# Kernel tuning notes

Measured on AMD Instinct MI355X. Metric: run time of the kernel, lower is better.

Reference implementation:

```python
import jax, jax.numpy as jnp
import numpy as np

N_MODULES = 8
AG_HIDDEN = 512
N_HID = 512
OUT_SIZE = 10
BATCH = 8192


def _state_mask(n_modules, n0, n1):
    # torch: eye(M).repeat_interleave(n0, 0).repeat_interleave(n1, 1)
    m = jnp.eye(n_modules, dtype=jnp.float32)
    return jnp.repeat(jnp.repeat(m, n0, axis=0), n1, axis=1)


def setup_inputs() -> dict:
    key = jax.random.key(0)
    ks = jax.random.split(key, 5)
    d_in = N_MODULES * AG_HIDDEN
    d_hid = N_MODULES * N_HID
    d_out = N_MODULES * OUT_SIZE
    s1 = 1.0 / np.sqrt(d_in)
    s2 = 1.0 / np.sqrt(d_hid)
    return {
        "x": jax.random.normal(ks[0], (BATCH, d_in), jnp.float32),
        "W1": jax.random.uniform(ks[1], (d_hid, d_in), jnp.float32, -s1, s1),
        "b1": jax.random.uniform(ks[2], (d_hid,), jnp.float32, -s1, s1),
        "W2": jax.random.uniform(ks[3], (d_out, d_hid), jnp.float32, -s2, s2),
        "b2": jax.random.uniform(ks[4], (d_out,), jnp.float32, -s2, s2),
    }


def reference(x, W1, b1, W2, b2):
    # block-diagonal masks (intra-module connectivity only)
    mask1 = _state_mask(N_MODULES, N_HID, AG_HIDDEN)   # [d_hid, d_in]
    mask2 = _state_mask(N_MODULES, OUT_SIZE, N_HID)    # [d_out, d_hid]
    h = jax.nn.relu(x @ (W1 * mask1).T + b1)           # [B, d_hid]
    y = h @ (W2 * mask2).T + b2                        # [B, d_out]
    # split(OUT_SIZE, -1) then stack on dim 1 == reshape to [B, n_modules, OUT_SIZE]
    return y.reshape(y.shape[0], N_MODULES, OUT_SIZE)
```

## Files before the change

kernel.cpp:

```cpp
#include <hip/hip_runtime.h>


#define NMOD 8
#define DIM 512
#define OSZ 10
#define BATCH 8192
#define D_IN 4096
#define D_OUT 80
#define BM 128
#define BN 256
#define BK 32

#define ASTRIDE 40
#define HSTRIDE 264
#define LDSA_SZ 5120
#define LDSB_SZ 8192

typedef __attribute__((ext_vector_type(8))) short short8;
typedef __attribute__((ext_vector_type(4))) float float4v;

__device__ __forceinline__ unsigned short f2bf(float f) {
    unsigned int u = __builtin_bit_cast(unsigned int, f);
    u += 0x7fffu + ((u >> 16) & 1u);
    return (unsigned short)(u >> 16);
}

__device__ __forceinline__ short8 cvt8(float4 a, float4 b) {
    short8 r;
    r[0] = (short)f2bf(a.x); r[1] = (short)f2bf(a.y); r[2] = (short)f2bf(a.z); r[3] = (short)f2bf(a.w);
    r[4] = (short)f2bf(b.x); r[5] = (short)f2bf(b.y); r[6] = (short)f2bf(b.z); r[7] = (short)f2bf(b.w);
    return r;
}

__global__ void init_out_kernel(const float* __restrict__ b2, float* __restrict__ out) {
    int idx = blockIdx.x * 256 + threadIdx.x;
    out[idx] = b2[idx % D_OUT];
}

__global__ void cvt_w_kernel(const float* __restrict__ W1, ushort* __restrict__ w1b) {
    int j = blockIdx.x * 256 + threadIdx.x;
    int mm = j >> 16, rem = j & 65535, r = rem >> 7, c4 = rem & 127;
    float4 v = *(const float4*)(W1 + (size_t)(mm * DIM + r) * D_IN + mm * DIM + c4 * 4);
    *(ushort4*)(w1b + (size_t)mm * DIM * DIM + r * DIM + c4 * 4) =
        make_ushort4(f2bf(v.x), f2bf(v.y), f2bf(v.z), f2bf(v.w));
}

template <bool WPRE>
__global__ __launch_bounds__(256, 2)
void fused_kernel(const float* __restrict__ x, const float* __restrict__ W1,
                  const ushort* __restrict__ w1b, const float* __restrict__ b1,
                  const float* __restrict__ W2, const float* __restrict__ b2,
                  float* __restrict__ out) {
    __shared__ __attribute__((aligned(16))) ushort smem[26624];
    ushort* ldsA0 = smem;
    ushort* ldsA1 = smem + LDSA_SZ;
    ushort* ldsB0 = smem + 2 * LDSA_SZ;
    ushort* ldsB1 = smem + 2 * LDSA_SZ + LDSB_SZ;
    ushort* ldsH  = smem;

    const int tid  = threadIdx.x;
    const int wave = tid >> 6;
    const int lane = tid & 63;
    const int r16  = lane & 15;
    const int kq   = lane >> 4;

    const int bid     = blockIdx.x;
    const int m       = bid & 7;
    const int half    = (bid >> 3) & 1;
    const int rowBase = (bid >> 4) * BM;

    const float*  xsrc = x + (size_t)rowBase * D_IN + m * DIM;
    const ushort* w1h  = w1b + (size_t)m * DIM * DIM + (size_t)half * BN * DIM;
    const float*  w1f  = W1 + (size_t)(m * DIM + half * BN) * D_IN + m * DIM;

    const int arow = tid >> 1;
    const int ah   = tid & 1;
    const int brow = tid >> 2;
    const int bc   = tid & 3;

    float4v acc[8][4];
#pragma unroll
    for (int i = 0; i < 8; i++)
#pragma unroll
        for (int j = 0; j < 4; j++) acc[i][j] = (float4v){0.f, 0.f, 0.f, 0.f};

    if (WPRE) {
#pragma unroll
        for (int r = 0; r < 4; r++) {
            const int row = r * 64 + brow;
            const int f   = (row >> 1) & 3;
            __builtin_amdgcn_global_load_lds(
                (const __attribute__((address_space(1))) void*)(w1h + (size_t)row * DIM + (bc ^ f) * 8),
                (__attribute__((address_space(3))) void*)(ldsB0 + row * BK + bc * 8), 16, 0, 0);
        }
    } else {
#pragma unroll
        for (int r = 0; r < 4; r++) {
            const int row = r * 64 + brow;
            const int f   = (row >> 1) & 3;
            const float* p = w1f + (size_t)row * D_IN + bc * 8;
            *(short8*)(ldsB0 + row * BK + (bc ^ f) * 8) = cvt8(*(const float4*)p, *(const float4*)(p + 4));
        }
    }
    {
        const float* p = xsrc + (size_t)arow * D_IN + ah * 16;
        float4 a0 = *(const float4*)p, a1 = *(const float4*)(p + 4);
        float4 a2 = *(const float4*)(p + 8), a3 = *(const float4*)(p + 12);
        *(short8*)(ldsA0 + arow * ASTRIDE + ah * 16)     = cvt8(a0, a1);
        *(short8*)(ldsA0 + arow * ASTRIDE + ah * 16 + 8) = cvt8(a2, a3);
    }

    for (int kk = 0; kk < DIM / BK; kk++) {
        __syncthreads();
        ushort* Ac = (kk & 1) ? ldsA1 : ldsA0;
        ushort* Bc = (kk & 1) ? ldsB1 : ldsB0;
        ushort* An = (kk & 1) ? ldsA0 : ldsA1;
        ushort* Bn = (kk & 1) ? ldsB0 : ldsB1;

        float4 xr0, xr1, xr2, xr3;
        const bool pf = (kk < DIM / BK - 1);
        if (pf) {
            const int k0n = (kk + 1) * BK;
            if (WPRE) {
#pragma unroll
                for (int r = 0; r < 4; r++) {
                    const int row = r * 64 + brow;
                    const int f   = (row >> 1) & 3;
                    __builtin_amdgcn_global_load_lds(
                        (const __attribute__((address_space(1))) void*)(w1h + (size_t)row * DIM + k0n + (bc ^ f) * 8),
                        (__attribute__((address_space(3))) void*)(Bn + row * BK + bc * 8), 16, 0, 0);
                }
            }
            const float* p = xsrc + (size_t)arow * D_IN + kk * BK + BK + ah * 16;
            xr0 = *(const float4*)p;     xr1 = *(const float4*)(p + 4);
            xr2 = *(const float4*)(p + 8); xr3 = *(const float4*)(p + 12);
        }

        short8 aF[8], bF[4];
#pragma unroll
        for (int mt = 0; mt < 8; mt++)
            aF[mt] = *(const short8*)(Ac + (mt * 16 + r16) * ASTRIDE + kq * 8);
#pragma unroll
        for (int nt = 0; nt < 4; nt++) {
            const int row = wave * 64 + nt * 16 + r16;
            bF[nt] = *(const short8*)(Bc + row * BK + (kq ^ ((row >> 1) & 3)) * 8);
        }
#pragma unroll
        for (int mt = 0; mt < 8; mt++)
#pragma unroll
            for (int nt = 0; nt < 4; nt++)
                acc[mt][nt] = __builtin_amdgcn_mfma_f32_16x16x32_bf16(aF[mt], bF[nt], acc[mt][nt], 0, 0, 0);

        if (pf) {
            *(short8*)(An + arow * ASTRIDE + ah * 16)     = cvt8(xr0, xr1);
            *(short8*)(An + arow * ASTRIDE + ah * 16 + 8) = cvt8(xr2, xr3);
            if (!WPRE) {
#pragma unroll
                for (int r = 0; r < 4; r++) {
                    const int row = r * 64 + brow;
                    const int f   = (row >> 1) & 3;
                    const float* p = w1f + (size_t)row * D_IN + kk * BK + BK + bc * 8;
                    *(short8*)(Bn + row * BK + (bc ^ f) * 8) = cvt8(*(const float4*)p, *(const float4*)(p + 4));
                }
            }
        }
    }

    float b1v[4];
#pragma unroll
    for (int nt = 0; nt < 4; nt++)
        b1v[nt] = b1[m * DIM + half * BN + wave * 64 + nt * 16 + r16];

    for (int hh = 0; hh < 2; hh++) {
        __syncthreads();
#pragma unroll
        for (int mt2 = 0; mt2 < 4; mt2++) {
            const int mt = hh * 4 + mt2;
#pragma unroll
            for (int nt = 0; nt < 4; nt++) {
#pragma unroll
                for (int reg = 0; reg < 4; reg++) {
                    float v = acc[mt][nt][reg] + b1v[nt];
                    v = v > 0.f ? v : 0.f;
                    const int lr  = mt2 * 16 + kq * 4 + reg;
                    const int col = wave * 64 + nt * 16 + r16;
                    ldsH[lr * HSTRIDE + col] = f2bf(v);
                }
            }
        }
        __syncthreads();

        {
            float4v acc2 = (float4v){0.f, 0.f, 0.f, 0.f};
            const int hrow = wave * 16 + r16;
            const float* w2row = W2 + (size_t)(m * OSZ + r16) * D_IN + m * DIM + half * BN;
#pragma unroll
            for (int kc = 0; kc < BN / 32; kc++) {
                const int c = kc * 32 + kq * 8;
                short8 hA = *(const short8*)(ldsH + hrow * HSTRIDE + c);
                short8 wb = {0, 0, 0, 0, 0, 0, 0, 0};
                if (r16 < OSZ) {
                    const float* p = w2row + c;
                    wb = cvt8(*(const float4*)p, *(const float4*)(p + 4));
                }
                acc2 = __builtin_amdgcn_mfma_f32_16x16x32_bf16(hA, wb, acc2, 0, 0, 0);
            }
            if (r16 < OSZ) {
#pragma unroll
                for (int reg = 0; reg < 4; reg++) {
                    const int grow = rowBase + hh * 64 + wave * 16 + kq * 4 + reg;
                    atomicAdd(out + (size_t)grow * D_OUT + m * OSZ + r16, acc2[reg]);
                }
            }
        }
    }
}

extern "C" void kernel_launch(void* const* d_in, const int* in_sizes, int n_in,
                              void* d_out, int out_size, void* d_ws, size_t ws_size,
                              hipStream_t stream) {
    const float* x  = (const float*)d_in[0];
    const float* W1 = (const float*)d_in[1];
    const float* b1 = (const float*)d_in[2];
    const float* W2 = (const float*)d_in[3];
    const float* b2 = (const float*)d_in[4];
    float* out = (float*)d_out;

    init_out_kernel<<<dim3(2560), dim3(256), 0, stream>>>(b2, out);

    if (ws_size >= (size_t)NMOD * DIM * DIM * sizeof(ushort)) {
        ushort* w1b = (ushort*)d_ws;
        cvt_w_kernel<<<dim3(2048), dim3(256), 0, stream>>>(W1, w1b);
        fused_kernel<true><<<dim3(1024), dim3(256), 0, stream>>>(x, W1, w1b, b1, W2, b2, out);
    } else {
        fused_kernel<false><<<dim3(1024), dim3(256), 0, stream>>>(x, W1, nullptr, b1, W2, b2, out);
    }
}
```

Baseline: 260.4 us.

## Add software-pipelined fused kernel with async LDS weight loads and packed bf16 convert

Adds a new fused kernel for the precomputed-bf16-weight path. Each K step issues the next W1 tile with global_load_lds directly into XOR-swizzled LDS and prefetches the next x tile into registers before computing the current tile. Waits use explicit vmcnt and lgkmcnt counts, so memory latency can overlap with MFMA work. It also swaps the scalar f32-to-bf16 rounding for the v_cvt_pk_bf16_f32 instruction. The risks are fragile hand-placed waitcnts, higher register pressure from double-buffered x registers, and the inline-asm convert possibly rounding differently.

```diff
diff --git a/kernel.cpp b/kernel.cpp
--- a/kernel.cpp
+++ b/kernel.cpp
@@ -10,14 +10,23 @@
 #define BM 128
 #define BN 256
 #define BK 32
+#define NK (DIM / BK)
 
 #define ASTRIDE 40
 #define HSTRIDE 264
+#define A_SZ 5120
+#define B_SZ 8192
+
 #define LDSA_SZ 5120
 #define LDSB_SZ 8192
 
+#define VMCNT(n) asm volatile("s_waitcnt vmcnt(" #n ")" ::: "memory")
+#define LGKM0()  asm volatile("s_waitcnt lgkmcnt(0)" ::: "memory")
+#define MEMFENCE() asm volatile("" ::: "memory")
+
 typedef __attribute__((ext_vector_type(8))) short short8;
 typedef __attribute__((ext_vector_type(4))) float float4v;
+typedef __attribute__((ext_vector_type(4))) unsigned int uint4v;
 
 __device__ __forceinline__ unsigned short f2bf(float f) {
     unsigned int u = __builtin_bit_cast(unsigned int, f);
@@ -26,10 +35,13 @@
 }
 
 __device__ __forceinline__ short8 cvt8(float4 a, float4 b) {
-    short8 r;
-    r[0] = (short)f2bf(a.x); r[1] = (short)f2bf(a.y); r[2] = (short)f2bf(a.z); r[3] = (short)f2bf(a.w);
-    r[4] = (short)f2bf(b.x); r[5] = (short)f2bf(b.y); r[6] = (short)f2bf(b.z); r[7] = (short)f2bf(b.w);
-    return r;
+    unsigned int u0, u1, u2, u3;
+    asm("v_cvt_pk_bf16_f32 %0, %1, %2" : "=v"(u0) : "v"(a.x), "v"(a.y));
+    asm("v_cvt_pk_bf16_f32 %0, %1, %2" : "=v"(u1) : "v"(a.z), "v"(a.w));
+    asm("v_cvt_pk_bf16_f32 %0, %1, %2" : "=v"(u2) : "v"(b.x), "v"(b.y));
+    asm("v_cvt_pk_bf16_f32 %0, %1, %2" : "=v"(u3) : "v"(b.z), "v"(b.w));
+    uint4v u = {u0, u1, u2, u3};
+    return __builtin_bit_cast(short8, u);
 }
 
 __global__ void init_out_kernel(const float* __restrict__ b2, float* __restrict__ out) {
@@ -43,6 +55,178 @@
     float4 v = *(const float4*)(W1 + (size_t)(mm * DIM + r) * D_IN + mm * DIM + c4 * 4);
     *(ushort4*)(w1b + (size_t)mm * DIM * DIM + r * DIM + c4 * 4) =
         make_ushort4(f2bf(v.x), f2bf(v.y), f2bf(v.z), f2bf(v.w));
+}
+
+__global__ __launch_bounds__(256, 2)
+void fused_pipe(const float* __restrict__ x, const ushort* __restrict__ w1b,
+                const float* __restrict__ b1, const float* __restrict__ W2,
+                float* __restrict__ out) {
+    __shared__ __attribute__((aligned(16))) ushort smem[26624];
+    ushort* A0 = smem;
+    ushort* A1 = smem + A_SZ;
+    ushort* B0 = smem + 2 * A_SZ;
+    ushort* B1 = smem + 2 * A_SZ + B_SZ;
+    ushort* ldsH = smem;
+
+    const int tid  = threadIdx.x;
+    const int wave = tid >> 6;
+    const int lane = tid & 63;
+    const int r16  = lane & 15;
+    const int kq   = lane >> 4;
+
+    const int bid     = blockIdx.x;
+    const int m       = bid & 7;
+    const int half    = (bid >> 3) & 1;
+    const int rowBase = (bid >> 4) * BM;
+
+    const float*  xsrc = x + (size_t)rowBase * D_IN + m * DIM;
+    const ushort* w1h  = w1b + (size_t)m * DIM * DIM + (size_t)half * BN * DIM;
+
+    const int arow = tid >> 1;
+    const int ah   = tid & 1;
+    const int brow = tid >> 2;
+    const int bc   = tid & 3;
+
+    float4v acc[8][4];
+#pragma unroll
+    for (int i = 0; i < 8; i++)
+#pragma unroll
+        for (int j = 0; j < 4; j++) acc[i][j] = (float4v){0.f, 0.f, 0.f, 0.f};
+
+    float4 xrA[4], xrB[4];
+
+    auto issueX = [&](int k, float4 (&xr)[4]) {
+        const float* p = xsrc + (size_t)arow * D_IN + k * BK + ah * 16;
+        xr[0] = *(const float4*)p;       xr[1] = *(const float4*)(p + 4);
+        xr[2] = *(const float4*)(p + 8); xr[3] = *(const float4*)(p + 12);
+    };
+    auto issueW = [&](int k, ushort* Bn) {
+#pragma unroll
+        for (int r = 0; r < 4; r++) {
+            const int row = r * 64 + brow;
+            const int f   = (row >> 1) & 3;
+            __builtin_amdgcn_global_load_lds(
+                (const __attribute__((address_space(1))) void*)(w1h + (size_t)row * DIM + k * BK + (bc ^ f) * 8),
+                (__attribute__((address_space(3))) void*)(Bn + row * BK + bc * 8), 16, 0, 0);
+        }
+    };
+    auto writeA = [&](float4 (&xr)[4], ushort* An) {
+        *(short8*)(An + arow * ASTRIDE + ah * 16)     = cvt8(xr[0], xr[1]);
+        *(short8*)(An + arow * ASTRIDE + ah * 16 + 8) = cvt8(xr[2], xr[3]);
+    };
+    auto compute = [&](const ushort* Ac, const ushort* Bc) {
+        short8 aF[8], bF[4];
+#pragma unroll
+        for (int mt = 0; mt < 8; mt++)
+            aF[mt] = *(const short8*)(Ac + (mt * 16 + r16) * ASTRIDE + kq * 8);
+#pragma unroll
+        for (int nt = 0; nt < 4; nt++) {
+            const int row = wave * 64 + nt * 16 + r16;
+            bF[nt] = *(const short8*)(Bc + row * BK + (kq ^ ((row >> 1) & 3)) * 8);
+        }
+#pragma unroll
+        for (int mt = 0; mt < 8; mt++)
+#pragma unroll
+            for (int nt = 0; nt < 4; nt++)
+                acc[mt][nt] = __builtin_amdgcn_mfma_f32_16x16x32_bf16(aF[mt], bF[nt], acc[mt][nt], 0, 0, 0);
+    };
+
+    issueX(0, xrA);  MEMFENCE();
+    issueW(0, B0);   MEMFENCE();
+    issueX(1, xrB);
+    VMCNT(4);
+    writeA(xrA, A0);
+    LGKM0();
+    __builtin_amdgcn_s_barrier();
+    MEMFENCE();
+
+    for (int k2 = 0; k2 < 14; k2 += 2) {
+        {
+            issueW(k2 + 1, B1);  MEMFENCE();
+            issueX(k2 + 2, xrA); MEMFENCE();
+            compute(A0, B0);
+            MEMFENCE();
+            VMCNT(4);
+            writeA(xrB, A1);
+            LGKM0();
+            __builtin_amdgcn_s_barrier();
+            MEMFENCE();
+        }
+        {
+            issueW(k2 + 2, B0);  MEMFENCE();
+            issueX(k2 + 3, xrB); MEMFENCE();
+            compute(A1, B1);
+            MEMFENCE();
+            VMCNT(4);
+            writeA(xrA, A0);
+            LGKM0();
+            __builtin_amdgcn_s_barrier();
+            MEMFENCE();
+        }
+    }
+    {
+        issueW(15, B1);  MEMFENCE();
+        compute(A0, B0);
+        MEMFENCE();
+        VMCNT(0);
+        writeA(xrB, A1);
+        LGKM0();
+        __builtin_amdgcn_s_barrier();
+        MEMFENCE();
+    }
+    {
+        compute(A1, B1);
+        MEMFENCE();
+    }
+
+    float b1v[4];
+#pragma unroll
+    for (int nt = 0; nt < 4; nt++)
+        b1v[nt] = b1[m * DIM + half * BN + wave * 64 + nt * 16 + r16];
+
+    for (int hh = 0; hh < 2; hh++) {
+        __syncthreads();
+#pragma unroll
+        for (int mt2 = 0; mt2 < 4; mt2++) {
+            const int mt = hh * 4 + mt2;
+#pragma unroll
+            for (int nt = 0; nt < 4; nt++) {
+#pragma unroll
+                for (int reg = 0; reg < 4; reg++) {
+                    float v = acc[mt][nt][reg] + b1v[nt];
+                    v = v > 0.f ? v : 0.f;
+                    const int lr  = mt2 * 16 + kq * 4 + reg;
+                    const int col = wave * 64 + nt * 16 + r16;
+                    ldsH[lr * HSTRIDE + col] = f2bf(v);
+                }
+            }
+        }
+        __syncthreads();
+
+        {
+            float4v acc2 = (float4v){0.f, 0.f, 0.f, 0.f};
+            const int hrow = wave * 16 + r16;
+            const float* w2row = W2 + (size_t)(m * OSZ + r16) * D_IN + m * DIM + half * BN;
+#pragma unroll
+            for (int kc = 0; kc < BN / 32; kc++) {
+                const int c = kc * 32 + kq * 8;
+                short8 hA = *(const short8*)(ldsH + hrow * HSTRIDE + c);
+                short8 wb = {0, 0, 0, 0, 0, 0, 0, 0};
+                if (r16 < OSZ) {
+                    const float* p = w2row + c;
+                    wb = cvt8(*(const float4*)p, *(const float4*)(p + 4));
+                }
+                acc2 = __builtin_amdgcn_mfma_f32_16x16x32_bf16(hA, wb, acc2, 0, 0, 0);
+            }
+            if (r16 < OSZ) {
+#pragma unroll
+                for (int reg = 0; reg < 4; reg++) {
+                    const int grow = rowBase + hh * 64 + wave * 16 + kq * 4 + reg;
+                    atomicAdd(out + (size_t)grow * D_OUT + m * OSZ + r16, acc2[reg]);
+                }
+            }
+        }
+    }
 }
 
 template <bool WPRE>
@@ -231,7 +415,7 @@
     if (ws_size >= (size_t)NMOD * DIM * DIM * sizeof(ushort)) {
         ushort* w1b = (ushort*)d_ws;
         cvt_w_kernel<<<dim3(2048), dim3(256), 0, stream>>>(W1, w1b);
-        fused_kernel<true><<<dim3(1024), dim3(256), 0, stream>>>(x, W1, w1b, b1, W2, b2, out);
+        fused_pipe<<<dim3(1024), dim3(256), 0, stream>>>(x, w1b, b1, W2, out);
     } else {
         fused_kernel<false><<<dim3(1024), dim3(256), 0, stream>>>(x, W1, nullptr, b1, W2, b2, out);
     }
```

Result: no change. 258.3 us (-0.8%).

## Pre-swizzle W1 into MFMA fragment order and compute full hidden row per block

Applied to the files above, without the earlier changes.

The weight-conversion kernel now writes W1 in bf16, already arranged in per-lane MFMA fragment order, so the main kernel loads B fragments straight from global memory into registers with double buffering instead of staging them through LDS. Each block now handles 64 rows across the full 512-wide hidden dimension and keeps the whole converted x tile in LDS. Because every output element then has a single writer, the second GEMM stores results directly with the bias, which removes the init kernel and the atomics. Conversion uses the packed v_cvt_pk_bf16_f32 instruction. The trade-offs are that B fragments are re-read from global/L2 by every block, and the 64KB LDS tile may limit occupancy.

```diff
diff --git a/kernel.cpp b/kernel.cpp
--- a/kernel.cpp
+++ b/kernel.cpp
@@ -7,17 +7,18 @@
 #define BATCH 8192
 #define D_IN 4096
 #define D_OUT 80
-#define BM 128
-#define BN 256
-#define BK 32
-
-#define ASTRIDE 40
-#define HSTRIDE 264
+#define BM 64
+#define NK 16
+#define NGRAN (NMOD * 16 * 4 * 8 * 64)
+
 #define LDSA_SZ 5120
 #define LDSB_SZ 8192
+#define HSTRIDE 264
 
 typedef __attribute__((ext_vector_type(8))) short short8;
 typedef __attribute__((ext_vector_type(4))) float float4v;
+typedef __attribute__((ext_vector_type(4))) unsigned int uint4v;
+typedef __attribute__((ext_vector_type(2))) unsigned int uint2v;
 
 __device__ __forceinline__ unsigned short f2bf(float f) {
     unsigned int u = __builtin_bit_cast(unsigned int, f);
@@ -25,11 +26,15 @@
     return (unsigned short)(u >> 16);
 }
 
+__device__ __forceinline__ unsigned int pk2(float a, float b) {
+    unsigned int r;
+    asm("v_cvt_pk_bf16_f32 %0, %1, %2" : "=v"(r) : "v"(a), "v"(b));
+    return r;
+}
+
 __device__ __forceinline__ short8 cvt8(float4 a, float4 b) {
-    short8 r;
-    r[0] = (short)f2bf(a.x); r[1] = (short)f2bf(a.y); r[2] = (short)f2bf(a.z); r[3] = (short)f2bf(a.w);
-    r[4] = (short)f2bf(b.x); r[5] = (short)f2bf(b.y); r[6] = (short)f2bf(b.z); r[7] = (short)f2bf(b.w);
-    return r;
+    uint4v u = {pk2(a.x, a.y), pk2(a.z, a.w), pk2(b.x, b.y), pk2(b.z, b.w)};
+    return __builtin_bit_cast(short8, u);
 }
 
 __global__ void init_out_kernel(const float* __restrict__ b2, float* __restrict__ out) {
@@ -37,19 +42,140 @@
     out[idx] = b2[idx % D_OUT];
 }
 
-__global__ void cvt_w_kernel(const float* __restrict__ W1, ushort* __restrict__ w1b) {
+__global__ void cvt_w_kernel(const float* __restrict__ W1, ushort* __restrict__ wb2) {
     int j = blockIdx.x * 256 + threadIdx.x;
-    int mm = j >> 16, rem = j & 65535, r = rem >> 7, c4 = rem & 127;
-    float4 v = *(const float4*)(W1 + (size_t)(mm * DIM + r) * D_IN + mm * DIM + c4 * 4);
-    *(ushort4*)(w1b + (size_t)mm * DIM * DIM + r * DIM + c4 * 4) =
-        make_ushort4(f2bf(v.x), f2bf(v.y), f2bf(v.z), f2bf(v.w));
-}
-
-template <bool WPRE>
+    if (j >= NGRAN) return;
+    int r16 = j & 15, kq = (j >> 4) & 3;
+    int nt = (j >> 6) & 7, wc = (j >> 9) & 3, kk = (j >> 11) & 15, mm = j >> 15;
+    int col = wc * 128 + nt * 16 + r16;
+    int k   = kk * 32 + kq * 8;
+    const float* p = W1 + (size_t)(mm * DIM + col) * D_IN + mm * DIM + k;
+    *(short8*)(wb2 + (size_t)j * 8) = cvt8(*(const float4*)p, *(const float4*)(p + 4));
+}
+
+__global__ __launch_bounds__(256, 2)
+void fused_full(const float* __restrict__ x, const ushort* __restrict__ wb2,
+                const float* __restrict__ b1, const float* __restrict__ W2,
+                const float* __restrict__ b2, float* __restrict__ out) {
+    __shared__ __attribute__((aligned(16))) ushort xS[32768];
+
+    const int tid  = threadIdx.x;
+    const int wc   = tid >> 6;
+    const int lane = tid & 63;
+    const int r16  = lane & 15;
+    const int kq   = lane >> 4;
+
+    const int bid     = blockIdx.x;
+    const int m       = bid & 7;
+    const int rowBase = (bid >> 3) * BM;
+
+    {
+        const float* xbase = x + (size_t)(rowBase + wc * 16) * D_IN + m * DIM;
+#pragma unroll
+        for (int i = 0; i < 32; i++) {
+            const int r = i >> 1, h = i & 1;
+            const int row = wc * 16 + r;
+            const float* p = xbase + (size_t)r * D_IN + h * 256 + lane * 4;
+            float4 v = *(const float4*)p;
+            const int g = h * 32 + (lane >> 1);
+            const int addr = row * 512 + ((g ^ ((row & 1) << 2)) << 3) + ((lane & 1) << 2);
+            uint2v w = {pk2(v.x, v.y), pk2(v.z, v.w)};
+            *(uint2v*)(xS + addr) = w;
+        }
+    }
+    __syncthreads();
+
+    float b1v[8];
+#pragma unroll
+    for (int nt = 0; nt < 8; nt++)
+        b1v[nt] = b1[m * DIM + wc * 128 + nt * 16 + r16];
+
+    float4v acc[4][8];
+#pragma unroll
+    for (int i = 0; i < 4; i++)
+#pragma unroll
+        for (int j = 0; j < 8; j++) acc[i][j] = (float4v){0.f, 0.f, 0.f, 0.f};
+
+    const ushort* wbase = wb2 + (size_t)m * 16 * 16384 + wc * 4096 + lane * 8;
+    short8 bA[8], bB[8];
+
+    auto loadB = [&](int kk, short8 (&bf)[8]) {
+        const ushort* p = wbase + (size_t)kk * 16384;
+#pragma unroll
+        for (int nt = 0; nt < 8; nt++)
+            bf[nt] = *(const short8*)(p + nt * 512);
+    };
+    auto step = [&](int kk, short8 (&bf)[8]) {
+        short8 aF[4];
+#pragma unroll
+        for (int mt = 0; mt < 4; mt++) {
+            const int row  = mt * 16 + r16;
+            const int slot = (kk * 4 + kq) ^ ((r16 & 1) << 2);
+            aF[mt] = *(const short8*)(xS + row * 512 + slot * 8);
+        }
+#pragma unroll
+        for (int mt = 0; mt < 4; mt++)
+#pragma unroll
+            for (int nt = 0; nt < 8; nt++)
+                acc[mt][nt] = __builtin_amdgcn_mfma_f32_16x16x32_bf16(aF[mt], bf[nt], acc[mt][nt], 0, 0, 0);
+    };
+
+    loadB(0, bA);
+    for (int kk2 = 0; kk2 < NK; kk2 += 2) {
+        loadB(kk2 + 1, bB);
+        step(kk2, bA);
+        if (kk2 + 2 < NK) loadB(kk2 + 2, bA);
+        step(kk2 + 1, bB);
+    }
+
+    __syncthreads();
+    ushort* ldsH = xS;
+#pragma unroll
+    for (int mt = 0; mt < 4; mt++) {
+#pragma unroll
+        for (int nt = 0; nt < 8; nt++) {
+#pragma unroll
+            for (int reg = 0; reg < 4; reg++) {
+                float v = acc[mt][nt][reg] + b1v[nt];
+                v = v > 0.f ? v : 0.f;
+                const int row = mt * 16 + kq * 4 + reg;
+                const int col = wc * 128 + nt * 16 + r16;
+                const int g = col >> 3, c7 = col & 7;
+                ldsH[row * 512 + ((g ^ ((reg & 1) << 2)) << 3) + c7] = f2bf(v);
+            }
+        }
+    }
+    __syncthreads();
+
+    {
+        float4v acc2 = (float4v){0.f, 0.f, 0.f, 0.f};
+        const float* w2row = W2 + (size_t)(m * OSZ + r16) * D_IN + m * DIM;
+#pragma unroll
+        for (int kc = 0; kc < 16; kc++) {
+            const int row  = wc * 16 + r16;
+            const int slot = (kc * 4 + kq) ^ ((r16 & 1) << 2);
+            short8 hA = *(const short8*)(ldsH + row * 512 + slot * 8);
+            short8 wb = {0, 0, 0, 0, 0, 0, 0, 0};
+            if (r16 < OSZ) {
+                const float* p = w2row + kc * 32 + kq * 8;
+                wb = cvt8(*(const float4*)p, *(const float4*)(p + 4));
+            }
+            acc2 = __builtin_amdgcn_mfma_f32_16x16x32_bf16(hA, wb, acc2, 0, 0, 0);
+        }
+        if (r16 < OSZ) {
+            const float bias = b2[m * OSZ + r16];
+#pragma unroll
+            for (int reg = 0; reg < 4; reg++) {
+                const int grow = rowBase + wc * 16 + kq * 4 + reg;
+                out[(size_t)grow * D_OUT + m * OSZ + r16] = acc2[reg] + bias;
+            }
+        }
+    }
+}
+
 __global__ __launch_bounds__(256, 2)
 void fused_kernel(const float* __restrict__ x, const float* __restrict__ W1,
-                  const ushort* __restrict__ w1b, const float* __restrict__ b1,
-                  const float* __restrict__ W2, const float* __restrict__ b2,
+                  const float* __restrict__ b1, const float* __restrict__ W2,
                   float* __restrict__ out) {
     __shared__ __attribute__((aligned(16))) ushort smem[26624];
     ushort* ldsA0 = smem;
@@ -67,11 +193,10 @@
     const int bid     = blockIdx.x;
     const int m       = bid & 7;
     const int half    = (bid >> 3) & 1;
-    const int rowBase = (bid >> 4) * BM;
+    const int rowBase = (bid >> 4) * 128;
 
     const float*  xsrc = x + (size_t)rowBase * D_IN + m * DIM;
-    const ushort* w1h  = w1b + (size_t)m * DIM * DIM + (size_t)half * BN * DIM;
-    const float*  w1f  = W1 + (size_t)(m * DIM + half * BN) * D_IN + m * DIM;
+    const float*  w1f  = W1 + (size_t)(m * DIM + half * 256) * D_IN + m * DIM;
 
     const int arow = tid >> 1;
     const int ah   = tid & 1;
@@ -84,33 +209,22 @@
 #pragma unroll
         for (int j = 0; j < 4; j++) acc[i][j] = (float4v){0.f, 0.f, 0.f, 0.f};
 
-    if (WPRE) {
-#pragma unroll
-        for (int r = 0; r < 4; r++) {
-            const int row = r * 64 + brow;
-            const int f   = (row >> 1) & 3;
-            __builtin_amdgcn_global_load_lds(
-                (const __attribute__((address_space(1))) void*)(w1h + (size_t)row * DIM + (bc ^ f) * 8),
-                (__attribute__((address_space(3))) void*)(ldsB0 + row * BK + bc * 8), 16, 0, 0);
-        }
-    } else {
-#pragma unroll
-        for (int r = 0; r < 4; r++) {
-            const int row = r * 64 + brow;
-            const int f   = (row >> 1) & 3;
-            const float* p = w1f + (size_t)row * D_IN + bc * 8;
-            *(short8*)(ldsB0 + row * BK + (bc ^ f) * 8) = cvt8(*(const float4*)p, *(const float4*)(p + 4));
-        }
+#pragma unroll
+    for (int r = 0; r < 4; r++) {
+        const int row = r * 64 + brow;
+        const int f   = (row >> 1) & 3;
+        const float* p = w1f + (size_t)row * D_IN + bc * 8;
+        *(short8*)(ldsB0 + row * 32 + (bc ^ f) * 8) = cvt8(*(const float4*)p, *(const float4*)(p + 4));
     }
     {
         const float* p = xsrc + (size_t)arow * D_IN + ah * 16;
         float4 a0 = *(const float4*)p, a1 = *(const float4*)(p + 4);
         float4 a2 = *(const float4*)(p + 8), a3 = *(const float4*)(p + 12);
-        *(short8*)(ldsA0 + arow * ASTRIDE + ah * 16)     = cvt8(a0, a1);
-        *(short8*)(ldsA0 + arow * ASTRIDE + ah * 16 + 8) = cvt8(a2, a3);
-    }
-
-    for (int kk = 0; kk < DIM / BK; kk++) {
+        *(short8*)(ldsA0 + arow * 40 + ah * 16)     = cvt8(a0, a1);
+        *(short8*)(ldsA0 + arow * 40 + ah * 16 + 8) = cvt8(a2, a3);
+    }
+
+    for (int kk = 0; kk < 16; kk++) {
         __syncthreads();
         ushort* Ac = (kk & 1) ? ldsA1 : ldsA0;
         ushort* Bc = (kk & 1) ? ldsB1 : ldsB0;
@@ -118,20 +232,9 @@
         ushort* Bn = (kk & 1) ? ldsB0 : ldsB1;
 
         float4 xr0, xr1, xr2, xr3;
-        const bool pf = (kk < DIM / BK - 1);
+        const bool pf = (kk < 15);
         if (pf) {
-            const int k0n = (kk + 1) * BK;
-            if (WPRE) {
-#pragma unroll
-                for (int r = 0; r < 4; r++) {
-                    const int row = r * 64 + brow;
-                    const int f   = (row >> 1) & 3;
-                    __builtin_amdgcn_global_load_lds(
-                        (const __attribute__((address_space(1))) void*)(w1h + (size_t)row * DIM + k0n + (bc ^ f) * 8),
-                        (__attribute__((address_space(3))) void*)(Bn + row * BK + bc * 8), 16, 0, 0);
-                }
-            }
-            const float* p = xsrc + (size_t)arow * D_IN + kk * BK + BK + ah * 16;
+            const float* p = xsrc + (size_t)arow * D_IN + kk * 32 + 32 + ah * 16;
             xr0 = *(const float4*)p;     xr1 = *(const float4*)(p + 4);
             xr2 = *(const float4*)(p + 8); xr3 = *(const float4*)(p + 12);
         }
@@ -139,11 +242,11 @@
         short8 aF[8], bF[4];
 #pragma unroll
         for (int mt = 0; mt < 8; mt++)
-            aF[mt] = *(const short8*)(Ac + (mt * 16 + r16) * ASTRIDE + kq * 8);
+            aF[mt] = *(const short8*)(Ac + (mt * 16 + r16) * 40 + kq * 8);
 #pragma unroll
         for (int nt = 0; nt < 4; nt++) {
             const int row = wave * 64 + nt * 16 + r16;
-            bF[nt] = *(const short8*)(Bc + row * BK + (kq ^ ((row >> 1) & 3)) * 8);
+            bF[nt] = *(const short8*)(Bc + row * 32 + (kq ^ ((row >> 1) & 3)) * 8);
         }
 #pragma unroll
         for (int mt = 0; mt < 8; mt++)
@@ -152,16 +255,14 @@
                 acc[mt][nt] = __builtin_amdgcn_mfma_f32_16x16x32_bf16(aF[mt], bF[nt], acc[mt][nt], 0, 0, 0);
 
         if (pf) {
-            *(short8*)(An + arow * ASTRIDE + ah * 16)     = cvt8(xr0, xr1);
-            *(short8*)(An + arow * ASTRIDE + ah * 16 + 8) = cvt8(xr2, xr3);
-            if (!WPRE) {
-#pragma unroll
-                for (int r = 0; r < 4; r++) {
-                    const int row = r * 64 + brow;
-                    const int f   = (row >> 1) & 3;
-                    const float* p = w1f + (size_t)row * D_IN + kk * BK + BK + bc * 8;
-                    *(short8*)(Bn + row * BK + (bc ^ f) * 8) = cvt8(*(const float4*)p, *(const float4*)(p + 4));
-                }
+            *(short8*)(An + arow * 40 + ah * 16)     = cvt8(xr0, xr1);
+            *(short8*)(An + arow * 40 + ah * 16 + 8) = cvt8(xr2, xr3);
+#pragma unroll
+            for (int r = 0; r < 4; r++) {
+                const int row = r * 64 + brow;
+                const int f   = (row >> 1) & 3;
+                const float* p = w1f + (size_t)row * D_IN + kk * 32 + 32 + bc * 8;
+                *(short8*)(Bn + row * 32 + (bc ^ f) * 8) = cvt8(*(const float4*)p, *(const float4*)(p + 4));
             }
         }
     }
@@ -169,7 +270,7 @@
     float b1v[4];
 #pragma unroll
     for (int nt = 0; nt < 4; nt++)
-        b1v[nt] = b1[m * DIM + half * BN + wave * 64 + nt * 16 + r16];
+        b1v[nt] = b1[m * DIM + half * 256 + wave * 64 + nt * 16 + r16];
 
     for (int hh = 0; hh < 2; hh++) {
         __syncthreads();
@@ -193,9 +294,9 @@
         {
             float4v acc2 = (float4v){0.f, 0.f, 0.f, 0.f};
             const int hrow = wave * 16 + r16;
-            const float* w2row = W2 + (size_t)(m * OSZ + r16) * D_IN + m * DIM + half * BN;
-#pragma unroll
-            for (int kc = 0; kc < BN / 32; kc++) {
+            const float* w2row = W2 + (size_t)(m * OSZ + r16) * D_IN + m * DIM + half * 256;
+#pragma unroll
+            for (int kc = 0; kc < 8; kc++) {
                 const int c = kc * 32 + kq * 8;
                 short8 hA = *(const short8*)(ldsH + hrow * HSTRIDE + c);
                 short8 wb = {0, 0, 0, 0, 0, 0, 0, 0};
@@ -226,13 +327,12 @@
     const float* b2 = (const float*)d_in[4];
     float* out = (float*)d_out;
 
-    init_out_kernel<<<dim3(2560), dim3(256), 0, stream>>>(b2, out);
-
     if (ws_size >= (size_t)NMOD * DIM * DIM * sizeof(ushort)) {
-        ushort* w1b = (ushort*)d_ws;
-        cvt_w_kernel<<<dim3(2048), dim3(256), 0, stream>>>(W1, w1b);
-        fused_kernel<true><<<dim3(1024), dim3(256), 0, stream>>>(x, W1, w1b, b1, W2, b2, out);
+        ushort* wb2 = (ushort*)d_ws;
+        cvt_w_kernel<<<dim3(1024), dim3(256), 0, stream>>>(W1, wb2);
+        fused_full<<<dim3(1024), dim3(256), 0, stream>>>(x, wb2, b1, W2, b2, out);
     } else {
-        fused_kernel<false><<<dim3(1024), dim3(256), 0, stream>>>(x, W1, nullptr, b1, W2, b2, out);
-    }
-}
+        init_out_kernel<<<dim3(2560), dim3(256), 0, stream>>>(b2, out);
+        fused_kernel<<<dim3(1024), dim3(256), 0, stream>>>(x, W1, b1, W2, out);
+    }
+}
```

Result: slower. 275.2 us (+5.7%).
